# Optimization experiments

Measured on AMD Instinct MI355X. Metric: run time of the kernel, lower is better.

## Reference

```python
import jax, jax.numpy as jnp
import numpy as np

GATE_SLOPE = 10.0
ALPHA = 0.8


def setup_inputs() -> dict:
    key = jax.random.key(0)
    k0, k1, k2, k3, k4, k5 = jax.random.split(key, 6)
    B, I, O, NB = 512, 128, 64, 8
    x = jax.random.normal(k0, (B, I), dtype=jnp.float32)
    k = jax.random.uniform(k1, (I, O, NB), dtype=jnp.float32) * 2.0 + 0.5
    Ec = jax.random.uniform(k2, (I, O, NB), dtype=jnp.float32) * 2.0 + 0.5
    Ps = jax.random.uniform(k3, (I, O, NB), dtype=jnp.float32) * 1.5 + 0.5
    bias = jax.random.normal(k4, (I, O, NB), dtype=jnp.float32) * 0.1
    coef = jax.random.normal(k5, (I, O, NB), dtype=jnp.float32)
    return {"x": x, "k": k, "Ec": Ec, "Ps": Ps, "bias": bias, "coef": coef}


def reference(x, k, Ec, Ps, bias, coef):
    # x: [B, I]; params: [I, O, NB]
    xe = x[:, :, None, None]  # [B, I, 1, 1], broadcasts against [I, O, NB]
    # The torch loop writes prev_x = x_sample each iteration, so sample b sees
    # x[b-1] as prev (x[-1] = 0 from the initial buffer). branch_sign is never
    # written back, so branch_snap == 1 always. prev is detached in torch.
    prev = jnp.concatenate([jnp.zeros_like(xe[:1]), xe[:-1]], axis=0)
    prev = jax.lax.stop_gradient(prev)

    is_moving_up = jax.nn.sigmoid(GATE_SLOPE * (xe - prev))          # [B,I,1,1]
    crossed_pos = jax.nn.sigmoid(GATE_SLOPE * (xe - Ec))             # [B,I,O,NB]
    crossed_neg = jax.nn.sigmoid(GATE_SLOPE * (-xe - Ec))            # [B,I,O,NB]
    switch_up = is_moving_up * crossed_pos
    switch_lo = (1.0 - is_moving_up) * crossed_neg
    # target = su*1 + sl*(-1) + (1 - su - sl)*branch_snap, branch_snap = 1
    target = switch_up - switch_lo + (1.0 - switch_up - switch_lo)
    branch_momentum = ALPHA + (1.0 - ALPHA) * target                 # alpha*1 + (1-alpha)*target
    basis = Ps * jnp.tanh(k * (xe + Ec * branch_momentum)) + bias    # [B,I,O,NB]
    return jnp.einsum('bion,ion->bo', basis, coef)                   # sum over (I, NB)
```

## Files before the change

### kernel.cpp

```cpp
#include <hip/hip_runtime.h>


#define GATE_C 14.426950408889634f
#define TANH_C 2.8853900817779268f

constexpr int B = 512, I = 128, O = 64, NB = 8, BT = 32, TILES = 2;

__device__ __forceinline__ float sig_neg(float u) {
  return __builtin_amdgcn_rcpf(1.f + __builtin_amdgcn_exp2f(u));
}

__global__ __launch_bounds__(1024, 4) void fe_main(
    const float* __restrict__ x, const float* __restrict__ k,
    const float* __restrict__ Ec, const float* __restrict__ Ps,
    const float* __restrict__ bias, const float* __restrict__ coef,
    float* __restrict__ out)
{
  __shared__ float4 p_lds[I * NB];
  __shared__ float2 xc_lds[BT][I + 1];
  __shared__ float red[16];

  const int tid = threadIdx.x;
  const int o = blockIdx.y;
  const int bbase = blockIdx.x * (BT * TILES);

  {
    const int i = tid >> 3, nn = tid & 7;
    const int g = (i * O + o) * NB + nn;
    const float E = Ec[g], K = k[g], P = Ps[g], C = coef[g], Bs = bias[g];
    const float pc = P * C;
    p_lds[tid] = make_float4(E, E * GATE_C, K * TANH_C, pc);
    float pbase = fmaf(Bs, C, pc);
    #pragma unroll
    for (int m = 1; m < 64; m <<= 1) pbase += __shfl_xor(pbase, m);
    if ((tid & 63) == 0) red[tid >> 6] = pbase;
  }

  const int n  = tid & 7;
  const int ih = (tid >> 3) & 3;
  const int bl = tid >> 5;
  const float4* __restrict__ prow = p_lds + (ih * 32) * 8 + n;

  for (int t = 0; t < TILES; ++t) {
    const int b0 = bbase + t * BT;
    __syncthreads();

    for (int e = tid; e < BT * I; e += 1024) {
      const int xbl = e >> 7, xi = e & 127;
      const int bg = b0 + xbl;
      const float xv = x[bg * I + xi];
      const float pv = (bg == 0) ? 0.f : x[(bg - 1) * I + xi];
      const float c = -0.4f * sig_neg(GATE_C * (xv - pv));
      xc_lds[xbl][xi] = make_float2(xv, c);
    }
    __syncthreads();

    const float2* __restrict__ xrow = &xc_lds[bl][ih * 32];
    float acc = 0.f;
    #pragma unroll 4
    for (int it = 0; it < 32; ++it) {
      const float2 xc = xrow[it];
      const float4 p  = prow[it * 8];
      const float sg = sig_neg(fmaf(xc.x, GATE_C, p.y));
      const float bm = fmaf(xc.y, sg, 1.f);
      const float inner = fmaf(p.x, bm, xc.x);
      const float r = sig_neg(p.z * inner);
      acc = fmaf(p.w, r, acc);
    }

    acc += __shfl_xor(acc, 1);
    acc += __shfl_xor(acc, 2);
    acc += __shfl_xor(acc, 4);
    acc += __shfl_xor(acc, 8);
    acc += __shfl_xor(acc, 16);

    if ((tid & 31) == 0) {
      float base = 0.f;
      #pragma unroll
      for (int w = 0; w < 16; ++w) base += red[w];
      out[(b0 + bl) * O + o] = fmaf(-2.f, acc, base);
    }
  }
}

extern "C" void kernel_launch(void* const* d_in, const int* in_sizes, int n_in,
                              void* d_out, int out_size, void* d_ws, size_t ws_size,
                              hipStream_t stream) {
  const float* x    = (const float*)d_in[0];
  const float* k    = (const float*)d_in[1];
  const float* Ec   = (const float*)d_in[2];
  const float* Ps   = (const float*)d_in[3];
  const float* bias = (const float*)d_in[4];
  const float* coef = (const float*)d_in[5];
  float* out = (float*)d_out;

  dim3 grid(B / (BT * TILES), O);
  fe_main<<<grid, 1024, 0, stream>>>(x, k, Ec, Ps, bias, coef, out);
}
```

Baseline: 25.82 us.

## Pack two batch rows per thread with packed-FP32 math and factored gate exponentials

Each thread now handles two batch rows at once using float2 vector types, so FMAs and multiplies can map to packed FP32 instructions. The gate sigmoid exp2(GATE_C*(x-E)) is factored into exp2(GATE_C*x)*exp2(-GATE_C*E)-style products, with both factors precomputed into LDS, so the inner loop drops one transcendental. Hardware rcp is replaced by a bit-trick initial guess refined with Newton steps, and the thread-to-work mapping and LDS layouts change, adding a cross-wave reduction through LDS with an extra barrier. Precision risks: the exponential factorisation may overflow for large x or E, and the approximate reciprocals lose some accuracy.

```diff
diff --git a/kernel.cpp b/kernel.cpp
--- a/kernel.cpp
+++ b/kernel.cpp
@@ -4,10 +4,23 @@
 #define GATE_C 14.426950408889634f
 #define TANH_C 2.8853900817779268f
 
+typedef float f32x2 __attribute__((ext_vector_type(2)));
+typedef float f32x4 __attribute__((ext_vector_type(4)));
+typedef int   i32x2 __attribute__((ext_vector_type(2)));
+
 constexpr int B = 512, I = 128, O = 64, NB = 8, BT = 32, TILES = 2;
+constexpr int BP = BT / 2;
 
-__device__ __forceinline__ float sig_neg(float u) {
-  return __builtin_amdgcn_rcpf(1.f + __builtin_amdgcn_exp2f(u));
+__device__ __forceinline__ f32x2 pk_rcp1(f32x2 d) {
+  i32x2 yi = (i32x2)(0x7EF127EA) - __builtin_bit_cast(i32x2, d);
+  f32x2 y = __builtin_bit_cast(f32x2, yi);
+  return y * __builtin_elementwise_fma(-d, y, (f32x2)(2.f));
+}
+__device__ __forceinline__ f32x2 pk_rcp2(f32x2 d) {
+  i32x2 yi = (i32x2)(0x7EF127EA) - __builtin_bit_cast(i32x2, d);
+  f32x2 y = __builtin_bit_cast(f32x2, yi);
+  y = y * __builtin_elementwise_fma(-d, y, (f32x2)(2.f));
+  return y * __builtin_elementwise_fma(-d, y, (f32x2)(2.f));
 }
 
 __global__ __launch_bounds__(1024, 4) void fe_main(
@@ -16,69 +29,87 @@
     const float* __restrict__ bias, const float* __restrict__ coef,
     float* __restrict__ out)
 {
-  __shared__ float4 p_lds[I * NB];
-  __shared__ float2 xc_lds[BT][I + 1];
+  __shared__ f32x4 pl[I][NB];
+  __shared__ f32x4 xp[I][BP];
+  __shared__ f32x2 up[I][BP];
+  __shared__ f32x2 racc[16][8];
   __shared__ float red[16];
 
   const int tid = threadIdx.x;
-  const int o = blockIdx.y;
-  const int bbase = blockIdx.x * (BT * TILES);
+  const int o   = blockIdx.y;
+  const int n   = tid & 7;
+  const int bpl = (tid >> 3) & 7;
+  const int w   = tid >> 6;
+  const int bp  = ((tid >> 6) & 1) * 8 + bpl;
+  const int ih  = tid >> 7;
 
   {
     const int i = tid >> 3, nn = tid & 7;
     const int g = (i * O + o) * NB + nn;
     const float E = Ec[g], K = k[g], P = Ps[g], C = coef[g], Bs = bias[g];
     const float pc = P * C;
-    p_lds[tid] = make_float4(E, E * GATE_C, K * TANH_C, pc);
+    pl[i][nn] = (f32x4){E, __builtin_amdgcn_exp2f(GATE_C * E), K * TANH_C, pc};
     float pbase = fmaf(Bs, C, pc);
     #pragma unroll
     for (int m = 1; m < 64; m <<= 1) pbase += __shfl_xor(pbase, m);
-    if ((tid & 63) == 0) red[tid >> 6] = pbase;
+    if ((tid & 63) == 0) red[w] = pbase;
   }
 
-  const int n  = tid & 7;
-  const int ih = (tid >> 3) & 3;
-  const int bl = tid >> 5;
-  const float4* __restrict__ prow = p_lds + (ih * 32) * 8 + n;
-
   for (int t = 0; t < TILES; ++t) {
-    const int b0 = bbase + t * BT;
+    const int b0 = blockIdx.x * (BT * TILES) + t * BT;
     __syncthreads();
 
-    for (int e = tid; e < BT * I; e += 1024) {
-      const int xbl = e >> 7, xi = e & 127;
-      const int bg = b0 + xbl;
-      const float xv = x[bg * I + xi];
-      const float pv = (bg == 0) ? 0.f : x[(bg - 1) * I + xi];
-      const float c = -0.4f * sig_neg(GATE_C * (xv - pv));
-      xc_lds[xbl][xi] = make_float2(xv, c);
+    for (int e = tid; e < I * BP; e += 1024) {
+      const int bq = e & 15, i = e >> 4;
+      const int re = b0 + 2 * bq;
+      const float xe = x[re * I + i];
+      const float xo = x[(re + 1) * I + i];
+      const float xm = (re == 0) ? 0.f : x[(re - 1) * I + i];
+      const float ce = -0.4f * __builtin_amdgcn_rcpf(
+          1.f + __builtin_amdgcn_exp2f(GATE_C * (xe - xm)));
+      const float co = -0.4f * __builtin_amdgcn_rcpf(
+          1.f + __builtin_amdgcn_exp2f(GATE_C * (xo - xe)));
+      xp[i][bq] = (f32x4){xe, xo, ce, co};
+      up[i][bq] = (f32x2){__builtin_amdgcn_exp2f(GATE_C * xe),
+                          __builtin_amdgcn_exp2f(GATE_C * xo)};
     }
     __syncthreads();
 
-    const float2* __restrict__ xrow = &xc_lds[bl][ih * 32];
-    float acc = 0.f;
-    #pragma unroll 4
-    for (int it = 0; it < 32; ++it) {
-      const float2 xc = xrow[it];
-      const float4 p  = prow[it * 8];
-      const float sg = sig_neg(fmaf(xc.x, GATE_C, p.y));
-      const float bm = fmaf(xc.y, sg, 1.f);
-      const float inner = fmaf(p.x, bm, xc.x);
-      const float r = sig_neg(p.z * inner);
-      acc = fmaf(p.w, r, acc);
+    f32x2 acc = (f32x2)(0.f);
+    #pragma unroll
+    for (int it = 0; it < 16; ++it) {
+      const int i = ih * 16 + it;
+      const f32x4 p = pl[i][n];
+      const f32x4 q = xp[i][bp];
+      const f32x2 u = up[i][bp];
+      const f32x2 x2 = q.lo, c2 = q.hi;
+      const f32x2 d1 = __builtin_elementwise_fma(u, (f32x2)(p.y), (f32x2)(1.f));
+      const f32x2 sg = pk_rcp1(d1);
+      const f32x2 bm = __builtin_elementwise_fma(c2, sg, (f32x2)(1.f));
+      const f32x2 inr = __builtin_elementwise_fma((f32x2)(p.x), bm, x2);
+      const f32x2 tt = (f32x2)(p.z) * inr;
+      f32x2 e2;
+      e2.x = __builtin_amdgcn_exp2f(tt.x);
+      e2.y = __builtin_amdgcn_exp2f(tt.y);
+      const f32x2 r = pk_rcp2(e2 + (f32x2)(1.f));
+      acc = __builtin_elementwise_fma((f32x2)(p.w), r, acc);
     }
 
-    acc += __shfl_xor(acc, 1);
-    acc += __shfl_xor(acc, 2);
-    acc += __shfl_xor(acc, 4);
-    acc += __shfl_xor(acc, 8);
-    acc += __shfl_xor(acc, 16);
+    acc.x += __shfl_xor(acc.x, 1); acc.y += __shfl_xor(acc.y, 1);
+    acc.x += __shfl_xor(acc.x, 2); acc.y += __shfl_xor(acc.y, 2);
+    acc.x += __shfl_xor(acc.x, 4); acc.y += __shfl_xor(acc.y, 4);
+    if (n == 0) racc[w][bpl] = acc;
+    __syncthreads();
 
-    if ((tid & 31) == 0) {
+    if (tid < 16) {
+      f32x2 s = (f32x2)(0.f);
+      #pragma unroll
+      for (int q8 = 0; q8 < 8; ++q8) s += racc[q8 * 2 + (tid >> 3)][tid & 7];
       float base = 0.f;
       #pragma unroll
-      for (int w = 0; w < 16; ++w) base += red[w];
-      out[(b0 + bl) * O + o] = fmaf(-2.f, acc, base);
+      for (int q = 0; q < 16; ++q) base += red[q];
+      out[(b0 + 2 * tid) * O + o]     = fmaf(-2.f, s.x, base);
+      out[(b0 + 2 * tid + 1) * O + o] = fmaf(-2.f, s.y, base);
     }
   }
 }
```

After: 24.87 us. -3.7%, faster.
